# Performance work log

Hardware: AMD Instinct MI355X
Metric: run time of the kernel (lower is better)

Reference implementation:

```python
import jax, jax.numpy as jnp
import numpy as np

B, T, N, F_IN = 8, 288, 2000, 1
E, ID, H, K = 128, 16, 128, 20
FL = T // 2 + 1  # rfft length = in_len//2 + 1
EPS_NORM = 1e-12
EPS_LN = 1e-8


def setup_inputs() -> dict:
    key = jax.random.key(0)
    k0, k1, k2, k3, k4 = jax.random.split(key, 5)
    return {
        "x": jax.random.normal(k0, (B, T, N, F_IN), jnp.float32),
        "Ex": jax.random.normal(k1, (FL, E), jnp.float32),
        "nodes": jax.random.normal(k2, (N, ID), jnp.float32),
        "Wd": jax.random.normal(k3, (N, E + ID, H), jnp.float32),
        "Wxabs": jax.random.normal(k4, (H, H), jnp.float32),
    }


def reference(x, Ex, nodes, Wd, Wxabs):
    # [B,T,N,F] -> take feature 0 -> [B,N,T]
    xt = jnp.transpose(x[:, :, :, 0], (0, 2, 1))
    xf = jnp.abs(jnp.fft.rfft(xt, axis=-1))  # [B,N,FL]
    # F.normalize p=2 over dim=1 (nodes), then dim=2 (freq): x / max(||x||, eps)
    xf = xf / jnp.clip(jnp.sqrt(jnp.sum(xf * xf, axis=1, keepdims=True)), EPS_NORM)
    xf = xf / jnp.clip(jnp.sqrt(jnp.sum(xf * xf, axis=2, keepdims=True)), EPS_NORM)
    xe = jnp.matmul(xf, Ex)  # [B,N,E]
    # cat(): append static node identity embedding per batch element
    xk = jnp.concatenate(
        [xe, jnp.broadcast_to(nodes, (xe.shape[0], N, ID))], axis=-1
    )  # [B,N,E+ID]
    # per-node weight bmm: [N,B,E+ID] @ [N,E+ID,H] -> [B,N,H]
    x1 = jax.nn.relu(jnp.einsum('bnd,ndh->bnh', xk, Wd))
    # LayerNorm over last two dims [N,H], eps=1e-8, no affine
    mu = jnp.mean(x1, axis=(1, 2), keepdims=True)
    var = jnp.mean((x1 - mu) ** 2, axis=(1, 2), keepdims=True)
    x2 = (x1 - mu) / jnp.sqrt(var + EPS_LN)
    # dropout is identity at inference
    adp = jnp.einsum('bnh,hk->bnk', x2, Wxabs)  # convt
    adj = jnp.einsum('bnh,bmh->bnm', adp, x1)  # [B,N,N]
    adp = jax.nn.relu(adj)
    # dy_mask_graph: per-row topk over dim=2 (torch dim=1 of the [N,N] slice),
    # binary mask via scatter of ones, then elementwise mask
    _, idx = jax.lax.top_k(adp, K)  # [B,N,K]
    bi = jnp.arange(adp.shape[0])[:, None, None]
    ni = jnp.arange(N)[None, :, None]
    mask = jnp.zeros_like(adp).at[bi, ni, idx].set(1.0)
    adj_masked = adp * mask
    return jax.nn.softmax(adj_masked, axis=2)
```

## Files before the change

kernel.cpp:

```cpp
#include <hip/hip_runtime.h>
#include <math.h>

#define BB 8
#define TT 288
#define NN 2000
#define FLEN 145
#define EE 128
#define IDD 16
#define HH 128
#define DKK 144
#define KTOP 20

typedef _Float16 half8 __attribute__((ext_vector_type(8)));
typedef float f32x4 __attribute__((ext_vector_type(4)));
typedef unsigned short ushort_t;

#define OFF_TW  ((size_t)0)
#define SZ_TW   ((size_t)TT*FLEN*2)
#define OFF_XF  (OFF_TW + SZ_TW)
#define SZ_XF   ((size_t)BB*FLEN*NN)
#define OFF_ICN (OFF_XF + SZ_XF)
#define OFF_IRN (OFF_ICN + (size_t)BB*FLEN)
#define OFF_XE  (OFF_IRN + (size_t)BB*NN)
#define SZ_BNH  ((size_t)BB*NN*HH)
#define OFF_X1  (OFF_XE + SZ_BNH)
#define OFF_ADP (OFF_X1 + SZ_BNH)
#define OFF_CSW (OFF_ADP + SZ_BNH)
#define OFF_LNS (OFF_CSW + HH)
#define OFF_LNF (OFF_LNS + 16)

#define CACHE_W 2064
#define FUSED_LDS_BYTES ((16 * CACHE_W + 2 * 8 * 64) * 4)

__device__ __forceinline__ float wredSum(float v) {
#pragma unroll
  for (int o = 32; o > 0; o >>= 1) v += __shfl_down(v, o, 64);
  return v;
}
__device__ __forceinline__ float wredMax(float v) {
#pragma unroll
  for (int o = 32; o > 0; o >>= 1) v = fmaxf(v, __shfl_down(v, o, 64));
  return v;
}
__device__ __forceinline__ float wredSumAll(float v) {
#pragma unroll
  for (int o = 32; o > 0; o >>= 1) v += __shfl_xor(v, o, 64);
  return v;
}
__device__ __forceinline__ float wredMaxAll(float v) {
#pragma unroll
  for (int o = 32; o > 0; o >>= 1) v = fmaxf(v, __shfl_xor(v, o, 64));
  return v;
}

__device__ __forceinline__ void split16(float v, ushort_t& hi, ushort_t& lo) {
  _Float16 h = (_Float16)v;
  _Float16 l = (_Float16)(v - (float)h);
  union { _Float16 f; ushort_t u; } a, b;
  a.f = h; b.f = l;
  hi = a.u; lo = b.u;
}

__global__ void k_init(const float* __restrict__ Wx, float* __restrict__ csw,
                       float* __restrict__ lns) {
  int k = threadIdx.x;
  float s = 0.f;
  for (int h = 0; h < HH; ++h) s += Wx[h * HH + k];
  csw[k] = s;
  if (k < 16) lns[k] = 0.f;
}

__global__ void k_tw(float* __restrict__ tw) {
  int id = blockIdx.x * 256 + threadIdx.x;
  if (id >= TT * FLEN) return;
  int t = id / FLEN, f = id % FLEN;
  int r = (t * f) % TT;
  double th = -2.0 * 3.14159265358979323846 * (double)r / (double)TT;
  tw[2 * id]     = (float)cos(th);
  tw[2 * id + 1] = (float)sin(th);
}

__global__ void k_dft(const float* __restrict__ x, const float* __restrict__ tw,
                      float* __restrict__ xf) {
  __shared__ __align__(16) float Xs[16][128];
  __shared__ __align__(16) float TWs[16][32][2];
  const int b = blockIdx.z;
  const int f0 = blockIdx.y * 32;
  const int n0 = blockIdx.x * 128;
  const int tid = threadIdx.x;
  const int tn = tid & 31;
  const int tf = tid >> 5;
  float ar[4][4] = {}, ai[4][4] = {};
  for (int t0 = 0; t0 < TT; t0 += 16) {
    __syncthreads();
    for (int l = tid; l < 512; l += 256) {
      int row = l >> 5, q = l & 31;
      int n = n0 + q * 4;
      const float* src = x + ((size_t)b * TT + (t0 + row)) * NN + n;
      float4 v = make_float4(0, 0, 0, 0);
      if (n + 3 < NN) v = *(const float4*)src;
      else {
        if (n + 0 < NN) v.x = src[0];
        if (n + 1 < NN) v.y = src[1];
        if (n + 2 < NN) v.z = src[2];
        if (n + 3 < NN) v.w = src[3];
      }
      *(float4*)&Xs[row][q * 4] = v;
    }
    for (int l = tid; l < 512; l += 256) {
      int row = l >> 5, ff = l & 31;
      int f = f0 + ff;
      float2 cs = make_float2(0, 0);
      if (f < FLEN) cs = *(const float2*)&tw[((size_t)(t0 + row) * FLEN + f) * 2];
      *(float2*)&TWs[row][ff][0] = cs;
    }
    __syncthreads();
#pragma unroll 4
    for (int t = 0; t < 16; ++t) {
      float4 xv = *(float4*)&Xs[t][tn * 4];
      float xx[4] = {xv.x, xv.y, xv.z, xv.w};
      float4 p0 = *(float4*)&TWs[t][tf * 4][0];
      float4 p1 = *(float4*)&TWs[t][tf * 4 + 2][0];
      float c[4] = {p0.x, p0.z, p1.x, p1.z};
      float s[4] = {p0.y, p0.w, p1.y, p1.w};
#pragma unroll
      for (int i = 0; i < 4; ++i)
#pragma unroll
        for (int j = 0; j < 4; ++j) {
          ar[i][j] = fmaf(xx[j], c[i], ar[i][j]);
          ai[i][j] = fmaf(xx[j], s[i], ai[i][j]);
        }
    }
  }
#pragma unroll
  for (int i = 0; i < 4; ++i) {
    int f = f0 + tf * 4 + i;
    if (f >= FLEN) continue;
    float* dst = &xf[((size_t)b * FLEN + f) * NN];
    float o[4];
#pragma unroll
    for (int j = 0; j < 4; ++j)
      o[j] = sqrtf(ar[i][j] * ar[i][j] + ai[i][j] * ai[i][j]);
    int n = n0 + tn * 4;
    if (n + 3 < NN) *(float4*)&dst[n] = make_float4(o[0], o[1], o[2], o[3]);
    else {
#pragma unroll
      for (int j = 0; j < 4; ++j) if (n + j < NN) dst[n + j] = o[j];
    }
  }
}

__global__ void k_colnorm(const float* __restrict__ xf, float* __restrict__ icn) {
  __shared__ float sc[4];
  int bf = blockIdx.x;
  const float* rowp = xf + (size_t)bf * NN;
  float s = 0.f;
  for (int i = threadIdx.x; i < NN; i += 256) { float v = rowp[i]; s = fmaf(v, v, s); }
  s = wredSum(s);
  int lane = threadIdx.x & 63, w = threadIdx.x >> 6;
  if (lane == 0) sc[w] = s;
  __syncthreads();
  if (threadIdx.x == 0)
    icn[bf] = 1.f / fmaxf(sqrtf(sc[0] + sc[1] + sc[2] + sc[3]), 1e-12f);
}

__global__ void k_rownorm(const float* __restrict__ xf, const float* __restrict__ icn,
                          float* __restrict__ irn) {
  int b = blockIdx.y;
  int n = blockIdx.x * 256 + threadIdx.x;
  if (n >= NN) return;
  float s = 0.f;
  for (int f = 0; f < FLEN; ++f) {
    float v = xf[((size_t)b * FLEN + f) * NN + n] * icn[b * FLEN + f];
    s = fmaf(v, v, s);
  }
  irn[b * NN + n] = 1.f / fmaxf(sqrtf(s), 1e-12f);
}

__global__ void k_xe(const float* __restrict__ xf, const float* __restrict__ icn,
                     const float* __restrict__ irn, const float* __restrict__ Ex,
                     float* __restrict__ xe) {
  __shared__ __align__(16) float As[16][64];
  __shared__ __align__(16) float Bs[16][128];
  const int b = blockIdx.y;
  const int n0 = blockIdx.x * 64;
  const int tid = threadIdx.x;
  const int tn = tid >> 4, te = tid & 15;
  float acc[4][8] = {};
  for (int f0 = 0; f0 < 160; f0 += 16) {
    __syncthreads();
    {
      int kt = tid >> 4, q = tid & 15;
      int f = f0 + kt;
      int n = n0 + q * 4;
      float4 v = make_float4(0, 0, 0, 0);
      if (f < FLEN) {
        float ic = icn[b * FLEN + f];
        const float* src = &xf[((size_t)b * FLEN + f) * NN + n];
        if (n + 3 < NN) v = *(const float4*)src;
        else {
          if (n + 0 < NN) v.x = src[0];
          if (n + 1 < NN) v.y = src[1];
          if (n + 2 < NN) v.z = src[2];
          if (n + 3 < NN) v.w = src[3];
        }
        v.x *= ic; v.y *= ic; v.z *= ic; v.w *= ic;
      }
      *(float4*)&As[kt][q * 4] = v;
    }
    for (int l = tid; l < 512; l += 256) {
      int kt = l >> 5, q = l & 31;
      int f = f0 + kt;
      float4 v = make_float4(0, 0, 0, 0);
      if (f < FLEN) v = *(const float4*)&Ex[(size_t)f * EE + q * 4];
      *(float4*)&Bs[kt][q * 4] = v;
    }
    __syncthreads();
#pragma unroll
    for (int k = 0; k < 16; ++k) {
      float4 a  = *(float4*)&As[k][tn * 4];
      float4 b0 = *(float4*)&Bs[k][te * 4];
      float4 b1 = *(float4*)&Bs[k][64 + te * 4];
      float av[4] = {a.x, a.y, a.z, a.w};
      float bv[8] = {b0.x, b0.y, b0.z, b0.w, b1.x, b1.y, b1.z, b1.w};
#pragma unroll
      for (int i = 0; i < 4; ++i)
#pragma unroll
        for (int j = 0; j < 8; ++j)
          acc[i][j] = fmaf(av[i], bv[j], acc[i][j]);
    }
  }
#pragma unroll
  for (int i = 0; i < 4; ++i) {
    int n = n0 + tn * 4 + i;
    if (n >= NN) continue;
    float sc = irn[b * NN + n];
    float* dst = &xe[((size_t)b * NN + n) * EE];
    *(float4*)&dst[te * 4] =
        make_float4(acc[i][0] * sc, acc[i][1] * sc, acc[i][2] * sc, acc[i][3] * sc);
    *(float4*)&dst[64 + te * 4] =
        make_float4(acc[i][4] * sc, acc[i][5] * sc, acc[i][6] * sc, acc[i][7] * sc);
  }
}

__global__ void k_x1(const float* xe, const float* __restrict__ nodes,
                     const float* __restrict__ Wd, float* __restrict__ x1,
                     ushort_t* x1hl) {
  __shared__ __align__(16) float xk[8][DKK];
  __shared__ float red[4][32][33];
  const int n = blockIdx.x;
  const int tid = threadIdx.x;
  {
    int b = tid >> 5, q = tid & 31;
    *(float4*)&xk[b][q * 4] = *(const float4*)&xe[((size_t)b * NN + n) * EE + q * 4];
  }
  if (tid < 128) {
    int b = tid >> 4, i = tid & 15;
    xk[b][EE + i] = nodes[(size_t)n * IDD + i];
  }
  __syncthreads();
  const int h4 = tid & 31;
  const int dg = tid >> 5;
  float acc[8][4] = {};
  for (int d = dg; d < DKK; d += 8) {
    float4 wv = *(const float4*)&Wd[((size_t)n * DKK + d) * HH + h4 * 4];
#pragma unroll
    for (int b = 0; b < 8; ++b) {
      float xv = xk[b][d];
      acc[b][0] = fmaf(xv, wv.x, acc[b][0]);
      acc[b][1] = fmaf(xv, wv.y, acc[b][1]);
      acc[b][2] = fmaf(xv, wv.z, acc[b][2]);
      acc[b][3] = fmaf(xv, wv.w, acc[b][3]);
    }
  }
#pragma unroll
  for (int b = 0; b < 8; ++b)
#pragma unroll
    for (int j = 0; j < 4; ++j)
      acc[b][j] += __shfl_xor(acc[b][j], 32, 64);
  const int wv_ = tid >> 6, lane = tid & 63;
  if (lane < 32) {
#pragma unroll
    for (int b = 0; b < 8; ++b)
#pragma unroll
      for (int j = 0; j < 4; ++j)
        red[wv_][lane][b * 4 + j] = acc[b][j];
  }
  __syncthreads();
#pragma unroll
  for (int o = 0; o < 4; ++o) {
    int idx = tid + o * 256;
    int b = idx >> 7, h = idx & 127;
    float s = red[0][h >> 2][b * 4 + (h & 3)] + red[1][h >> 2][b * 4 + (h & 3)] +
              red[2][h >> 2][b * 4 + (h & 3)] + red[3][h >> 2][b * 4 + (h & 3)];
    s = fmaxf(s, 0.f);
    x1[((size_t)b * NN + n) * HH + h] = s;
    ushort_t hi, lo;
    split16(s, hi, lo);
    size_t base = ((size_t)b * NN + n) * 256;
    x1hl[base + h] = hi;
    x1hl[base + 128 + h] = lo;
  }
}

__global__ void k_ln_stats(const float* __restrict__ x1, float* __restrict__ lns) {
  __shared__ float sc[4], sc2[4];
  int b = blockIdx.y, chunk = blockIdx.x;
  const float* base = x1 + (size_t)b * NN * HH + (size_t)chunk * 8000;
  float s = 0.f, s2 = 0.f;
  for (int i = threadIdx.x; i < 8000; i += 256) {
    float v = base[i];
    s += v; s2 = fmaf(v, v, s2);
  }
  s = wredSum(s); s2 = wredSum(s2);
  int lane = threadIdx.x & 63, w = threadIdx.x >> 6;
  if (lane == 0) { sc[w] = s; sc2[w] = s2; }
  __syncthreads();
  if (threadIdx.x == 0) {
    atomicAdd(&lns[b], sc[0] + sc[1] + sc[2] + sc[3]);
    atomicAdd(&lns[8 + b], sc2[0] + sc2[1] + sc2[2] + sc2[3]);
  }
}

__global__ void k_ln_final(const float* __restrict__ lns, float* __restrict__ lnf) {
  int b = threadIdx.x;
  if (b < 8) {
    float cnt = (float)(NN * HH);
    float mu = lns[b] / cnt;
    float var = fmaxf(lns[8 + b] / cnt - mu * mu, 0.f);
    lnf[b] = mu;
    lnf[8 + b] = 1.f / sqrtf(var + 1e-8f);
  }
}

__global__ void k_adp(const float* __restrict__ x1, const float* __restrict__ Wx,
                      const float* __restrict__ csw, const float* __restrict__ lnf,
                      ushort_t* __restrict__ adphl) {
  __shared__ __align__(16) float As[16][64];
  __shared__ __align__(16) float Bs[16][128];
  const int r0 = blockIdx.x * 64;
  const int tid = threadIdx.x;
  const int tn = tid >> 4, te = tid & 15;
  float acc[4][8] = {};
  for (int k0 = 0; k0 < HH; k0 += 16) {
    __syncthreads();
    {
      int rr = tid >> 2, kq = tid & 3;
      float4 v = *(const float4*)&x1[(size_t)(r0 + rr) * HH + k0 + kq * 4];
      As[kq * 4 + 0][rr] = v.x;
      As[kq * 4 + 1][rr] = v.y;
      As[kq * 4 + 2][rr] = v.z;
      As[kq * 4 + 3][rr] = v.w;
    }
    for (int l = tid; l < 512; l += 256) {
      int kt = l >> 5, q = l & 31;
      *(float4*)&Bs[kt][q * 4] = *(const float4*)&Wx[(size_t)(k0 + kt) * HH + q * 4];
    }
    __syncthreads();
#pragma unroll
    for (int k = 0; k < 16; ++k) {
      float4 a  = *(float4*)&As[k][tn * 4];
      float4 b0 = *(float4*)&Bs[k][te * 4];
      float4 b1 = *(float4*)&Bs[k][64 + te * 4];
      float av[4] = {a.x, a.y, a.z, a.w};
      float bv[8] = {b0.x, b0.y, b0.z, b0.w, b1.x, b1.y, b1.z, b1.w};
#pragma unroll
      for (int i = 0; i < 4; ++i)
#pragma unroll
        for (int j = 0; j < 8; ++j)
          acc[i][j] = fmaf(av[i], bv[j], acc[i][j]);
    }
  }
  float4 c0 = *(const float4*)&csw[te * 4];
  float4 c1 = *(const float4*)&csw[64 + te * 4];
  float cw[8] = {c0.x, c0.y, c0.z, c0.w, c1.x, c1.y, c1.z, c1.w};
#pragma unroll
  for (int i = 0; i < 4; ++i) {
    int r = r0 + tn * 4 + i;
    int b = r / NN;
    float mu = lnf[b], isd = lnf[8 + b];
    size_t base = (size_t)r * 256;
    ushort_t hi[8], lo[8];
#pragma unroll
    for (int j = 0; j < 8; ++j) {
      float o = (acc[i][j] - mu * cw[j]) * isd;
      split16(o, hi[j], lo[j]);
    }
    ushort4 u;
    u.x = hi[0]; u.y = hi[1]; u.z = hi[2]; u.w = hi[3];
    *(ushort4*)&adphl[base + te * 4] = u;
    u.x = hi[4]; u.y = hi[5]; u.z = hi[6]; u.w = hi[7];
    *(ushort4*)&adphl[base + 64 + te * 4] = u;
    u.x = lo[0]; u.y = lo[1]; u.z = lo[2]; u.w = lo[3];
    *(ushort4*)&adphl[base + 128 + te * 4] = u;
    u.x = lo[4]; u.y = lo[5]; u.z = lo[6]; u.w = lo[7];
    *(ushort4*)&adphl[base + 128 + 64 + te * 4] = u;
  }
}

__global__ __launch_bounds__(512, 1) void k_fused(
    const ushort_t* __restrict__ adphl, const ushort_t* __restrict__ x1hl,
    float* __restrict__ out) {
  extern __shared__ float smem[];
  float* cache = smem;
  float* scrV = smem + 16 * CACHE_W;
  int*   scrI = (int*)(scrV + 8 * 64);

  const int b = blockIdx.y;
  const int n0 = blockIdx.x * 16;
  const int tid = threadIdx.x;
  const int w = tid >> 6;
  const int lane = tid & 63;
  const int quad = lane >> 4, r16 = lane & 15;

  half8 Ah[4], Al[4];
  {
    const ushort_t* abase =
        adphl + ((size_t)(b * NN + n0 + r16)) * 256 + quad * 8;
#pragma unroll
    for (int ks = 0; ks < 4; ++ks) {
      Ah[ks] = *(const half8*)(abase + ks * 32);
      Al[ks] = *(const half8*)(abase + 128 + ks * 32);
    }
  }
  for (int s = 0; s < 4; ++s) {
    const int mb = s * 512 + w * 64;
#pragma unroll
    for (int i = 0; i < 4; ++i) {
      const int mt = mb + i * 16 + r16;
      const int mc = (mt < NN) ? mt : NN - 1;
      const ushort_t* bbase =
          x1hl + ((size_t)(b * NN + mc)) * 256 + quad * 8;
      half8 Bh[4], Bl[4];
#pragma unroll
      for (int ks = 0; ks < 4; ++ks) {
        Bh[ks] = *(const half8*)(bbase + ks * 32);
        Bl[ks] = *(const half8*)(bbase + 128 + ks * 32);
      }
      f32x4 acc = (f32x4){0.f, 0.f, 0.f, 0.f};
#pragma unroll
      for (int ks = 0; ks < 4; ++ks) {
        acc = __builtin_amdgcn_mfma_f32_16x16x32_f16(Ah[ks], Bh[ks], acc, 0, 0, 0);
        acc = __builtin_amdgcn_mfma_f32_16x16x32_f16(Ah[ks], Bl[ks], acc, 0, 0, 0);
        acc = __builtin_amdgcn_mfma_f32_16x16x32_f16(Al[ks], Bh[ks], acc, 0, 0, 0);
      }
#pragma unroll
      for (int reg = 0; reg < 4; ++reg) {
        int row = quad * 4 + reg;
        float v = (mt < NN) ? fmaxf(acc[reg], 0.f) : -1.f;
        cache[row * CACHE_W + mt] = v;
      }
    }
  }
  __syncthreads();

  for (int rr = 0; rr < 2; ++rr) {
    const int row = w * 2 + rr;
    const float* crow = cache + row * CACHE_W;
    f32x4 V[8];
#pragma unroll
    for (int j = 0; j < 8; ++j)
      V[j] = *(const f32x4*)&crow[j * 256 + lane * 4];

    float mx = -1.f, cp = 0.f;
#pragma unroll
    for (int j = 0; j < 8; ++j)
#pragma unroll
      for (int e = 0; e < 4; ++e) {
        mx = fmaxf(mx, V[j][e]);
        cp += (V[j][e] > 0.f) ? 1.f : 0.f;
      }
    const float m = wredMaxAll(mx);
    const float cpos = wredSumAll(cp);
    const float em = expf(-m);
    float* g = out + ((size_t)(b * NN + n0 + row)) * NN;

    if (cpos <= 20.5f) {
      float s = 0.f;
#pragma unroll
      for (int j = 0; j < 8; ++j)
#pragma unroll
        for (int e = 0; e < 4; ++e)
          if (V[j][e] > 0.f) s += expf(V[j][e] - m);
      s = wredSumAll(s);
      const float invD = 1.f / (s + (2000.f - cpos) * em);
      const float defv = em * invD;
#pragma unroll
      for (int j = 0; j < 8; ++j) {
        int m0 = j * 256 + lane * 4;
        if (m0 >= NN) continue;
        float4 o;
        o.x = (V[j][0] > 0.f) ? expf(V[j][0] - m) * invD : defv;
        o.y = (V[j][1] > 0.f) ? expf(V[j][1] - m) * invD : defv;
        o.z = (V[j][2] > 0.f) ? expf(V[j][2] - m) * invD : defv;
        o.w = (V[j][3] > 0.f) ? expf(V[j][3] - m) * invD : defv;
        *(float4*)&g[m0] = o;
      }
    } else {
      float tval = 0.f, cf = cpos;
      if (cpos > 64.5f) {
        float tlo = 0.f, thi = m;
        bool found = false;
        for (int it = 0; it < 64 && !found; ++it) {
          float mid = (it < 12)
              ? 0.5f * (tlo + thi)
              : __uint_as_float((__float_as_uint(tlo) + __float_as_uint(thi)) >> 1);
          float c = 0.f;
#pragma unroll
          for (int j = 0; j < 8; ++j)
#pragma unroll
            for (int e = 0; e < 4; ++e)
              c += (V[j][e] > mid) ? 1.f : 0.f;
          c = wredSumAll(c);
          if (c > 64.5f) tlo = mid;
          else if (c < 19.5f) thi = mid;
          else { tval = mid; cf = c; found = true; }
        }
        if (!found) { tval = tlo; cf = 64.f; }
      }
      int cI = (int)(cf + 0.5f);
      if (cI > 64) cI = 64;

      float* sv = scrV + w * 64;
      int* si = scrI + w * 64;
      int base = 0;
#pragma unroll
      for (int j = 0; j < 8; ++j)
#pragma unroll
        for (int e = 0; e < 4; ++e) {
          bool p = V[j][e] > tval;
          unsigned long long msk = __ballot(p);
          if (p) {
            int pos = base + (int)__popcll(msk & ((1ull << lane) - 1ull));
            if (pos < 64) { sv[pos] = V[j][e]; si[pos] = j * 256 + lane * 4 + e; }
          }
          base += (int)__popcll(msk);
        }
      asm volatile("s_waitcnt lgkmcnt(0)" ::: "memory");

      float cv = (lane < cI) ? sv[lane] : -1.f;
      int ci = (lane < cI) ? si[lane] : 0x7fffffff;
#pragma unroll
      for (int k = 2; k <= 64; k <<= 1)
#pragma unroll
        for (int j = k >> 1; j > 0; j >>= 1) {
          float ov = __shfl_xor(cv, j, 64);
          int oi = __shfl_xor(ci, j, 64);
          bool otherBetter = (ov > cv) || (ov == cv && oi < ci);
          bool iAmLow = (lane & j) == 0;
          bool desc = (lane & k) == 0;
          bool take = (desc == iAmLow) ? otherBetter : !otherBetter;
          if (take) { cv = ov; ci = oi; }
        }
      const float t20 = __shfl(cv, 19, 64);
      float e20 = (lane < 20) ? expf(cv - m) : 0.f;
      const float s20 = wredSumAll(e20);
      const float invD = 1.f / (s20 + (2000.f - 20.f) * em);
      const float defv = em * invD;
#pragma unroll
      for (int j = 0; j < 8; ++j) {
        int m0 = j * 256 + lane * 4;
        if (m0 >= NN) continue;
        float4 o;
        o.x = (V[j][0] >= t20) ? expf(V[j][0] - m) * invD : defv;
        o.y = (V[j][1] >= t20) ? expf(V[j][1] - m) * invD : defv;
        o.z = (V[j][2] >= t20) ? expf(V[j][2] - m) * invD : defv;
        o.w = (V[j][3] >= t20) ? expf(V[j][3] - m) * invD : defv;
        *(float4*)&g[m0] = o;
      }
    }
  }
}

extern "C" void kernel_launch(void* const* d_in, const int* in_sizes, int n_in,
                              void* d_out, int out_size, void* d_ws, size_t ws_size,
                              hipStream_t stream) {
  const float* x     = (const float*)d_in[0];
  const float* Ex    = (const float*)d_in[1];
  const float* nodes = (const float*)d_in[2];
  const float* Wd    = (const float*)d_in[3];
  const float* Wx    = (const float*)d_in[4];
  float* out = (float*)d_out;
  float* w = (float*)d_ws;
  float* tw  = w + OFF_TW;
  float* xf  = w + OFF_XF;
  float* icn = w + OFF_ICN;
  float* irn = w + OFF_IRN;
  float* xe  = w + OFF_XE;
  float* x1  = w + OFF_X1;
  float* csw = w + OFF_CSW;
  float* lns = w + OFF_LNS;
  float* lnf = w + OFF_LNF;
  ushort_t* adphl = (ushort_t*)(w + OFF_ADP);
  ushort_t* x1hl  = (ushort_t*)(w + OFF_XE);

  static int _once = []() {
    (void)hipFuncSetAttribute((const void*)k_fused,
                              hipFuncAttributeMaxDynamicSharedMemorySize,
                              FUSED_LDS_BYTES);
    return 0;
  }();
  (void)_once;

  k_init<<<1, 128, 0, stream>>>(Wx, csw, lns);
  k_tw<<<(TT * FLEN + 255) / 256, 256, 0, stream>>>(tw);
  k_dft<<<dim3(16, 5, BB), 256, 0, stream>>>(x, tw, xf);
  k_colnorm<<<BB * FLEN, 256, 0, stream>>>(xf, icn);
  k_rownorm<<<dim3(8, BB), 256, 0, stream>>>(xf, icn, irn);
  k_xe<<<dim3(32, BB), 256, 0, stream>>>(xf, icn, irn, Ex, xe);
  k_x1<<<NN, 256, 0, stream>>>(xe, nodes, Wd, x1, x1hl);
  k_ln_stats<<<dim3(32, BB), 256, 0, stream>>>(x1, lns);
  k_ln_final<<<1, 64, 0, stream>>>(lns, lnf);
  k_adp<<<250, 256, 0, stream>>>(x1, Wx, csw, lnf, adphl);
  k_fused<<<dim3(125, BB), 512, FUSED_LDS_BYTES, stream>>>(adphl, x1hl, out);
}
```

Baseline: 582.2 us.

## Double the fused block to 1024 threads and software-pipeline B-tile loads

The fused adjacency/top-k kernel now launches 16 waves per block instead of 8. Each wave computes 128 contiguous columns and then handles one output row instead of two. The B-operand loads are double-buffered so the next 16-column tile is fetched while the current tile's MFMAs run, to hide global load latency. The cost is higher register pressure under 1024-thread launch bounds, which could cause spills, and slightly more LDS for the scratch area.

```diff
diff --git a/kernel.cpp b/kernel.cpp
--- a/kernel.cpp
+++ b/kernel.cpp
@@ -30,7 +30,7 @@
 #define OFF_LNF (OFF_LNS + 16)
 
 #define CACHE_W 2064
-#define FUSED_LDS_BYTES ((16 * CACHE_W + 2 * 8 * 64) * 4)
+#define FUSED_LDS_BYTES ((16 * CACHE_W + 2 * 16 * 64) * 4)
 
 __device__ __forceinline__ float wredSum(float v) {
 #pragma unroll
@@ -398,13 +398,13 @@
   }
 }
 
-__global__ __launch_bounds__(512, 1) void k_fused(
+__global__ __launch_bounds__(1024, 1) void k_fused(
     const ushort_t* __restrict__ adphl, const ushort_t* __restrict__ x1hl,
     float* __restrict__ out) {
   extern __shared__ float smem[];
   float* cache = smem;
   float* scrV = smem + 16 * CACHE_W;
-  int*   scrI = (int*)(scrV + 8 * 64);
+  int*   scrI = (int*)(scrV + 16 * 64);
 
   const int b = blockIdx.y;
   const int n0 = blockIdx.x * 16;
@@ -423,39 +423,56 @@
       Al[ks] = *(const half8*)(abase + 128 + ks * 32);
     }
   }
-  for (int s = 0; s < 4; ++s) {
-    const int mb = s * 512 + w * 64;
-#pragma unroll
-    for (int i = 0; i < 4; ++i) {
-      const int mt = mb + i * 16 + r16;
-      const int mc = (mt < NN) ? mt : NN - 1;
-      const ushort_t* bbase =
-          x1hl + ((size_t)(b * NN + mc)) * 256 + quad * 8;
-      half8 Bh[4], Bl[4];
-#pragma unroll
-      for (int ks = 0; ks < 4; ++ks) {
-        Bh[ks] = *(const half8*)(bbase + ks * 32);
-        Bl[ks] = *(const half8*)(bbase + 128 + ks * 32);
-      }
-      f32x4 acc = (f32x4){0.f, 0.f, 0.f, 0.f};
-#pragma unroll
-      for (int ks = 0; ks < 4; ++ks) {
-        acc = __builtin_amdgcn_mfma_f32_16x16x32_f16(Ah[ks], Bh[ks], acc, 0, 0, 0);
-        acc = __builtin_amdgcn_mfma_f32_16x16x32_f16(Ah[ks], Bl[ks], acc, 0, 0, 0);
-        acc = __builtin_amdgcn_mfma_f32_16x16x32_f16(Al[ks], Bh[ks], acc, 0, 0, 0);
-      }
-#pragma unroll
-      for (int reg = 0; reg < 4; ++reg) {
-        int row = quad * 4 + reg;
-        float v = (mt < NN) ? fmaxf(acc[reg], 0.f) : -1.f;
-        cache[row * CACHE_W + mt] = v;
-      }
-    }
-  }
+  const int mbase = w * 128;
+
+  half8 Bh0[4], Bl0[4], Bh1[4], Bl1[4];
+
+#define LOADB(I, BH, BL)                                                      \
+  {                                                                           \
+    int mt_ = mbase + (I) * 16 + r16;                                         \
+    int mc_ = (mt_ < NN) ? mt_ : NN - 1;                                      \
+    const ushort_t* bb_ = x1hl + ((size_t)(b * NN + mc_)) * 256 + quad * 8;   \
+    BH[0] = *(const half8*)(bb_);       BL[0] = *(const half8*)(bb_ + 128);   \
+    BH[1] = *(const half8*)(bb_ + 32);  BL[1] = *(const half8*)(bb_ + 160);   \
+    BH[2] = *(const half8*)(bb_ + 64);  BL[2] = *(const half8*)(bb_ + 192);   \
+    BH[3] = *(const half8*)(bb_ + 96);  BL[3] = *(const half8*)(bb_ + 224);   \
+  }
+
+#define STEP(I, BH, BL, BH2, BL2)                                             \
+  {                                                                           \
+    if ((I) < 7) LOADB((I) + 1, BH2, BL2);                                    \
+    f32x4 acc = (f32x4){0.f, 0.f, 0.f, 0.f};                                  \
+    _Pragma("unroll")                                                         \
+    for (int ks = 0; ks < 4; ++ks) {                                          \
+      acc = __builtin_amdgcn_mfma_f32_16x16x32_f16(Ah[ks], BH[ks], acc, 0, 0, 0); \
+      acc = __builtin_amdgcn_mfma_f32_16x16x32_f16(Ah[ks], BL[ks], acc, 0, 0, 0); \
+      acc = __builtin_amdgcn_mfma_f32_16x16x32_f16(Al[ks], BH[ks], acc, 0, 0, 0); \
+    }                                                                         \
+    int mt_ = mbase + (I) * 16 + r16;                                         \
+    _Pragma("unroll")                                                         \
+    for (int reg = 0; reg < 4; ++reg) {                                       \
+      int row_ = quad * 4 + reg;                                              \
+      float v_ = (mt_ < NN) ? fmaxf(acc[reg], 0.f) : -1.f;                    \
+      cache[row_ * CACHE_W + mt_] = v_;                                       \
+    }                                                                         \
+  }
+
+  LOADB(0, Bh0, Bl0);
+  STEP(0, Bh0, Bl0, Bh1, Bl1);
+  STEP(1, Bh1, Bl1, Bh0, Bl0);
+  STEP(2, Bh0, Bl0, Bh1, Bl1);
+  STEP(3, Bh1, Bl1, Bh0, Bl0);
+  STEP(4, Bh0, Bl0, Bh1, Bl1);
+  STEP(5, Bh1, Bl1, Bh0, Bl0);
+  STEP(6, Bh0, Bl0, Bh1, Bl1);
+  STEP(7, Bh1, Bl1, Bh0, Bl0);
+#undef STEP
+#undef LOADB
+
   __syncthreads();
 
-  for (int rr = 0; rr < 2; ++rr) {
-    const int row = w * 2 + rr;
+  {
+    const int row = w;
     const float* crow = cache + row * CACHE_W;
     f32x4 V[8];
 #pragma unroll
@@ -612,5 +629,5 @@
   k_ln_stats<<<dim3(32, BB), 256, 0, stream>>>(x1, lns);
   k_ln_final<<<1, 64, 0, stream>>>(lns, lnf);
   k_adp<<<250, 256, 0, stream>>>(x1, Wx, csw, lnf, adphl);
-  k_fused<<<dim3(125, BB), 512, FUSED_LDS_BYTES, stream>>>(adphl, x1hl, out);
-}
+  k_fused<<<dim3(125, BB), 1024, FUSED_LDS_BYTES, stream>>>(adphl, x1hl, out);
+}
```

Result: no change. 571.5 us (-1.8%).
